# Optimization experiments

Hardware: AMD Instinct MI355X
Metric: run time of the kernel (lower is better)

Reference implementation:

```python
import jax, jax.numpy as jnp
import numpy as np

N_TOKENS = 4096
BATCH = 32


def setup_inputs() -> dict:
    key = jax.random.key(0)
    ks = jax.random.split(key, 9)
    n = N_TOKENS
    s = 0.02  # small init scale so exp(q*k) stays stable
    inp = {
        "x": jax.random.normal(ks[0], (BATCH, n), dtype=jnp.float32),
        "Wq": s * jax.random.normal(ks[1], (n, n), dtype=jnp.float32),
        "bq": jnp.zeros((n,), dtype=jnp.float32),
        "Wk": s * jax.random.normal(ks[2], (n, n), dtype=jnp.float32),
        "bk": jnp.zeros((n,), dtype=jnp.float32),
        "Wv": s * jax.random.normal(ks[3], (n, n), dtype=jnp.float32),
        "bv": jnp.zeros((n,), dtype=jnp.float32),
        "Wp": s * jax.random.normal(ks[4], (n, n), dtype=jnp.float32),
        "bp": jnp.zeros((n,), dtype=jnp.float32),
    }
    return inp


def reference(x, Wq, bq, Wk, bk, Wv, bv, Wp, bp):
    # Linear layers (torch convention: y = x @ W.T + b)
    q = x @ Wq.T + bq  # [b, n]
    k = x @ Wk.T + bk  # [b, n]
    v = x @ Wv.T + bv  # [b, n]
    # Rank-1 attention: scores[b,i,j] = q_i * k_j, softmax over j
    scores = q[:, :, None] * k[:, None, :]  # [b, n, n]
    w = jax.nn.softmax(scores, axis=2)
    attended = jnp.einsum('bij,bj->bi', w, v)  # [b, n]
    h = jax.nn.silu(x + attended)
    out = jax.nn.silu(h + h @ Wp.T + bp)
    return out
```

## Files before the change

kernel.cpp:

```cpp
#include <hip/hip_runtime.h>
#include <math.h>

#define N 4096
#define BATCH 32

#define NB 64
#define NP 9
#define QLO (-10.0f)
#define QBW 0.3125f
#define QINVBW 3.2f
#define NMOM (NB * 2 * NP)
#define NCHUNK 8

typedef short bf16x8 __attribute__((ext_vector_type(8)));
typedef float f32x4  __attribute__((ext_vector_type(4)));

static __device__ __forceinline__ float fast_exp2(float x) {
#if __has_builtin(__builtin_amdgcn_exp2f)
  return __builtin_amdgcn_exp2f(x);
#else
  return exp2f(x);
#endif
}

static __device__ __forceinline__ unsigned short f2bf_rne(float f) {
  unsigned int u = __float_as_uint(f);
  return (unsigned short)((u + 0x7FFFu + ((u >> 16) & 1u)) >> 16);
}
static __device__ __forceinline__ float bf2f(unsigned short h) {
  return __uint_as_float((unsigned int)h << 16);
}

__device__ const float c_invfact[NP] = {
  1.f, 1.f, 0.5f, 1.f/6.f, 1.f/24.f, 1.f/120.f, 1.f/720.f, 1.f/5040.f, 1.f/40320.f};

__global__ __launch_bounds__(256)
void prep_frags(const float* __restrict__ src, short* __restrict__ dst)
{
  int id = blockIdx.x * 256 + threadIdx.x;
  int narr = id >> 13;
  int rem  = id & 8191;
  int T = rem >> 6;
  int l = rem & 63;
  int b = (l & 15) | ((narr & 1) << 4);
  int k = T * 32 + ((l >> 4) << 3);
  const float* s = &src[(size_t)b * N + k];
  bf16x8 o;
  #pragma unroll
  for (int j = 0; j < 8; ++j) {
    float f = s[j];
    unsigned short h = f2bf_rne(f);
    if (narr >> 1) h = f2bf_rne(f - bf2f(h));
    o[j] = (short)h;
  }
  *(bf16x8*)&dst[(size_t)id * 8] = o;
}

template <int NSTEP, int NWAVES>
__device__ __forceinline__ void gemm_mfma_body(
    const float* __restrict__ W, const short* __restrict__ Xf,
    float* __restrict__ Y, int kbeg)
{
  const int t = threadIdx.x;
  const int w = t >> 6, l = t & 63;
  const int i0 = blockIdx.x * 16;

  const float* wrow = &W[(size_t)(i0 + (l & 15)) * N + kbeg + w * (NSTEP * 32) + ((l >> 4) << 3)];
  const short* bbase = Xf + (size_t)((kbeg >> 5) + w * NSTEP) * 512 + l * 8;

  f32x4 acc0 = {0.f, 0.f, 0.f, 0.f};
  f32x4 acc1 = {0.f, 0.f, 0.f, 0.f};

  #pragma unroll 4
  for (int s = 0; s < NSTEP; ++s) {
    float4 wa = *(const float4*)(wrow + s * 32);
    float4 wb = *(const float4*)(wrow + s * 32 + 4);
    bf16x8 bh0 = *(const bf16x8*)(bbase + (size_t)s * 512);
    bf16x8 bh1 = *(const bf16x8*)(bbase + (size_t)s * 512 + 65536);
    bf16x8 bl0 = *(const bf16x8*)(bbase + (size_t)s * 512 + 131072);
    bf16x8 bl1 = *(const bf16x8*)(bbase + (size_t)s * 512 + 196608);
    bf16x8 ah, al;
    #pragma unroll
    for (int e = 0; e < 8; ++e) {
      float x = (e < 4) ? ((const float*)&wa)[e] : ((const float*)&wb)[e - 4];
      unsigned int u = __float_as_uint(x);
      ah[e] = (short)(u >> 16);
      float r = x - __uint_as_float(u & 0xFFFF0000u);
      al[e] = (short)(__float_as_uint(r) >> 16);
    }
    acc0 = __builtin_amdgcn_mfma_f32_16x16x32_bf16(ah, bh0, acc0, 0, 0, 0);
    acc1 = __builtin_amdgcn_mfma_f32_16x16x32_bf16(ah, bh1, acc1, 0, 0, 0);
    acc0 = __builtin_amdgcn_mfma_f32_16x16x32_bf16(ah, bl0, acc0, 0, 0, 0);
    acc1 = __builtin_amdgcn_mfma_f32_16x16x32_bf16(ah, bl1, acc1, 0, 0, 0);
    acc0 = __builtin_amdgcn_mfma_f32_16x16x32_bf16(al, bh0, acc0, 0, 0, 0);
    acc1 = __builtin_amdgcn_mfma_f32_16x16x32_bf16(al, bh1, acc1, 0, 0, 0);
  }

  __shared__ float red[NWAVES][2][4][64];
  #pragma unroll
  for (int r = 0; r < 4; ++r) { red[w][0][r][l] = acc0[r]; red[w][1][r][l] = acc1[r]; }
  __syncthreads();

  #pragma unroll
  for (int e = t; e < 512; e += NWAVES * 64) {
    int b  = e >> 4;
    int il = e & 15;
    int n  = b >> 4;
    int lw = (b & 15) | ((il >> 2) << 4);
    int r  = il & 3;
    float v = 0.f;
    #pragma unroll
    for (int w2 = 0; w2 < NWAVES; ++w2) v += red[w2][n][r][lw];
    Y[(size_t)b * N + i0 + il] = v;
  }
}

__global__ __launch_bounds__(512) __attribute__((amdgpu_waves_per_eu(8)))
void gemm3(const short* __restrict__ Xf,
           const float* __restrict__ W0, const float* __restrict__ W1,
           const float* __restrict__ W2, float* __restrict__ GP)
{
  int m = blockIdx.y >> 1;
  const float* W = (m == 0) ? W0 : (m == 1) ? W1 : W2;
  gemm_mfma_body<8, 8>(W, Xf, GP + (size_t)blockIdx.y * (BATCH * N), (blockIdx.y & 1) * 2048);
}

__global__ __launch_bounds__(512) __attribute__((amdgpu_waves_per_eu(8)))
void gemm_p(const short* __restrict__ Hf, const float* __restrict__ W,
            float* __restrict__ GP)
{
  gemm_mfma_body<4, 8>(W, Hf, GP + (size_t)blockIdx.y * (BATCH * N), blockIdx.y * 1024);
}

__global__ __launch_bounds__(1024, 2)
void moments_a(const float* __restrict__ GP, const float* __restrict__ bk,
               const float* __restrict__ bv, float* __restrict__ P)
{
  const int b = blockIdx.x, chunk = blockIdx.y;
  const int t = threadIdx.x;
  const int wv = t >> 6, m = t & 63;

  __shared__ float ksm[512], vsm[512];
  {
    const float* GP2 = GP + (size_t)2 * BATCH * N;
    const float* GP3 = GP + (size_t)3 * BATCH * N;
    const float* GP4 = GP + (size_t)4 * BATCH * N;
    const float* GP5 = GP + (size_t)5 * BATCH * N;
    int col = chunk * 512 + (t & 511);
    size_t o = (size_t)b * N + col;
    if (t < 512) ksm[t] = GP2[o] + GP3[o] + bk[col];
    else         vsm[t & 511] = GP4[o] + GP5[o] + bv[col];
  }
  __syncthreads();

  const float gam = QLO + ((float)m + 0.5f) * QBW;
  const float gl2e = gam * 1.44269504f;
  float S[NP], T[NP];
  #pragma unroll
  for (int p = 0; p < NP; ++p) { S[p] = 0.f; T[p] = 0.f; }
  const int jb = wv * 32;
  #pragma unroll 4
  for (int jj = 0; jj < 32; ++jj) {
    float kj = ksm[jb + jj];
    float vj = vsm[jb + jj];
    float e = fast_exp2(gl2e * kj);
    float tp = e;
    S[0] += tp; T[0] = fmaf(tp, vj, T[0]);
    #pragma unroll
    for (int p = 1; p < NP; ++p) { tp *= kj; S[p] += tp; T[p] = fmaf(tp, vj, T[p]); }
  }
  __shared__ float red[16][NMOM];
  #pragma unroll
  for (int p = 0; p < NP; ++p) {
    red[wv][m * 18 + p] = S[p];
    red[wv][m * 18 + NP + p] = T[p];
  }
  __syncthreads();
  for (int e = t; e < NMOM; e += 1024) {
    float s = 0.f;
    #pragma unroll
    for (int w2 = 0; w2 < 16; ++w2) s += red[w2][e];
    P[((size_t)b * NCHUNK + chunk) * NMOM + e] = s;
  }
}

__global__ __launch_bounds__(256)
void attn_eval(const float* __restrict__ GP, const float* __restrict__ bq,
               const float* __restrict__ P, const float* __restrict__ x,
               float* __restrict__ h, short* __restrict__ Hf)
{
  const int b = blockIdx.x;
  const int i = blockIdx.y * 256 + threadIdx.x;
  __shared__ float cm[NMOM];
  for (int e = threadIdx.x; e < NMOM; e += 256) {
    float s = 0.f;
    #pragma unroll
    for (int c = 0; c < NCHUNK; ++c) s += P[((size_t)b * NCHUNK + c) * NMOM + e];
    int p = e % (2 * NP); if (p >= NP) p -= NP;
    cm[e] = s * c_invfact[p];
  }
  __syncthreads();
  size_t o = (size_t)b * N + i;
  float qv = GP[o] + GP[(size_t)BATCH * N + o] + bq[i];
  float qc = fminf(fmaxf(qv, QLO + 0.01f), -QLO - 0.01f);
  int m = (int)((qc - QLO) * QINVBW);
  float gam = QLO + ((float)m + 0.5f) * QBW;
  float d = qv - gam;
  const float* Sp = &cm[m * 18];
  float f = Sp[NP - 1], g = Sp[2 * NP - 1];
  #pragma unroll
  for (int p = NP - 2; p >= 0; --p) {
    f = fmaf(f, d, Sp[p]);
    g = fmaf(g, d, Sp[NP + p]);
  }
  float att = g / f;
  float z = x[o] + att;
  float hv = z / (1.f + fast_exp2(-1.44269504f * z));
  h[o] = hv;
  unsigned short hi = f2bf_rne(hv);
  unsigned short lo = f2bf_rne(hv - bf2f(hi));
  size_t base = (size_t)(b >> 4) * 65536 + (size_t)(i >> 5) * 512
              + (size_t)((b & 15) | (((i >> 3) & 3) << 4)) * 8 + (size_t)(i & 7);
  Hf[base] = (short)hi;
  Hf[base + 131072] = (short)lo;
}

__global__ __launch_bounds__(256)
void finalize_kernel(const float* __restrict__ h, const float* __restrict__ GP,
                     const float* __restrict__ bp, float* __restrict__ out)
{
  int idx = (blockIdx.x * 256 + threadIdx.x) * 4;
  int i = idx & (N - 1);
  const float* T0 = GP;
  const float* T1 = GP + (size_t)1 * BATCH * N;
  const float* T2 = GP + (size_t)2 * BATCH * N;
  const float* T3 = GP + (size_t)3 * BATCH * N;
  float4 hv = *(const float4*)&h[idx];
  float4 a  = *(const float4*)&T0[idx];
  float4 bb2 = *(const float4*)&T1[idx];
  float4 c  = *(const float4*)&T2[idx];
  float4 dd = *(const float4*)&T3[idx];
  float4 bb = *(const float4*)&bp[i];
  float4 z, o;
  z.x = hv.x + (a.x + bb2.x) + (c.x + dd.x) + bb.x;
  z.y = hv.y + (a.y + bb2.y) + (c.y + dd.y) + bb.y;
  z.z = hv.z + (a.z + bb2.z) + (c.z + dd.z) + bb.z;
  z.w = hv.w + (a.w + bb2.w) + (c.w + dd.w) + bb.w;
  o.x = z.x / (1.f + fast_exp2(-1.44269504f * z.x));
  o.y = z.y / (1.f + fast_exp2(-1.44269504f * z.y));
  o.z = z.z / (1.f + fast_exp2(-1.44269504f * z.z));
  o.w = z.w / (1.f + fast_exp2(-1.44269504f * z.w));
  *(float4*)&out[idx] = o;
}

extern "C" void kernel_launch(void* const* d_in, const int* in_sizes, int n_in,
                              void* d_out, int out_size, void* d_ws, size_t ws_size,
                              hipStream_t stream)
{
  const float* x  = (const float*)d_in[0];
  const float* Wq = (const float*)d_in[1];
  const float* bq = (const float*)d_in[2];
  const float* Wk = (const float*)d_in[3];
  const float* bk = (const float*)d_in[4];
  const float* Wv = (const float*)d_in[5];
  const float* bv = (const float*)d_in[6];
  const float* Wp = (const float*)d_in[7];
  const float* bp = (const float*)d_in[8];
  float* out = (float*)d_out;

  float* GP = (float*)d_ws;
  float* h  = GP + (size_t)6 * BATCH * N;
  short* Xf = (short*)(h + BATCH * N);
  short* Hf = Xf + 262144;
  float* P  = (float*)(Hf + 262144);

  prep_frags<<<dim3(128), 256, 0, stream>>>(x, Xf);
  gemm3<<<dim3(256, 6), 512, 0, stream>>>(Xf, Wq, Wk, Wv, GP);
  moments_a<<<dim3(BATCH, NCHUNK), 1024, 0, stream>>>(GP, bk, bv, P);
  attn_eval<<<dim3(BATCH, 16), 256, 0, stream>>>(GP, bq, P, x, h, Hf);
  gemm_p<<<dim3(256, 4), 512, 0, stream>>>(Hf, Wp, GP);
  finalize_kernel<<<dim3(128), 256, 0, stream>>>(h, GP, bp, out);
}
```

Baseline: 285.3 us.

## Double-buffer weight tiles via async global-to-LDS loads and drop split-K partials

The GEMM body now streams 16x256 float weight tiles into a double-buffered LDS staging area using global_load_lds async copies, so the next tile loads while MFMAs run on the current one. Each block covers a longer K range (full K for QKV, half K for the projection), which halves the number of blocks and partial outputs. The bias is fused into the GEMM epilogue, and the downstream kernels read finished q/k/v directly instead of summing split-K partials. The cost is less block-level parallelism (768 and 512 blocks), a __syncthreads on every tile, and the loss of the waves_per_eu hint.

```diff
diff --git a/kernel.cpp b/kernel.cpp
--- a/kernel.cpp
+++ b/kernel.cpp
@@ -33,6 +33,21 @@
 
 __device__ const float c_invfact[NP] = {
   1.f, 1.f, 0.5f, 1.f/6.f, 1.f/24.f, 1.f/120.f, 1.f/720.f, 1.f/5040.f, 1.f/40320.f};
+
+#if __has_builtin(__builtin_amdgcn_global_load_lds)
+#define HAVE_ASYNC_LDS 1
+#else
+#define HAVE_ASYNC_LDS 0
+#endif
+static __device__ __forceinline__ void async_cp16(const float* g, float* lds_base, int lane) {
+#if HAVE_ASYNC_LDS
+  __builtin_amdgcn_global_load_lds(
+      (const __attribute__((address_space(1))) void*)g,
+      (__attribute__((address_space(3))) void*)lds_base, 16, 0, 0);
+#else
+  ((float4*)lds_base)[lane] = *(const float4*)g;
+#endif
+}
 
 __global__ __launch_bounds__(256)
 void prep_frags(const float* __restrict__ src, short* __restrict__ dst)
@@ -56,33 +71,49 @@
   *(bf16x8*)&dst[(size_t)id * 8] = o;
 }
 
-template <int NSTEP, int NWAVES>
+template <int NTILE, bool FINAL>
 __device__ __forceinline__ void gemm_mfma_body(
     const float* __restrict__ W, const short* __restrict__ Xf,
-    float* __restrict__ Y, int kbeg)
-{
+    const float* __restrict__ bias, float* __restrict__ Y, int kbeg)
+{
+  __shared__ __align__(16) union GSm {
+    float stg[2][16][256];
+    float red[8][2][4][64];
+  } sm;
   const int t = threadIdx.x;
   const int w = t >> 6, l = t & 63;
   const int i0 = blockIdx.x * 16;
 
-  const float* wrow = &W[(size_t)(i0 + (l & 15)) * N + kbeg + w * (NSTEP * 32) + ((l >> 4) << 3)];
-  const short* bbase = Xf + (size_t)((kbeg >> 5) + w * NSTEP) * 512 + l * 8;
+  const float* gsrc0 = &W[(size_t)(i0 + 2 * w)     * N + kbeg + 4 * l];
+  const float* gsrc1 = &W[(size_t)(i0 + 2 * w + 1) * N + kbeg + 4 * l];
+  const short* bbase = Xf + (size_t)(kbeg >> 5) * 512 + l * 8;
 
   f32x4 acc0 = {0.f, 0.f, 0.f, 0.f};
   f32x4 acc1 = {0.f, 0.f, 0.f, 0.f};
 
-  #pragma unroll 4
-  for (int s = 0; s < NSTEP; ++s) {
-    float4 wa = *(const float4*)(wrow + s * 32);
-    float4 wb = *(const float4*)(wrow + s * 32 + 4);
-    bf16x8 bh0 = *(const bf16x8*)(bbase + (size_t)s * 512);
-    bf16x8 bh1 = *(const bf16x8*)(bbase + (size_t)s * 512 + 65536);
-    bf16x8 bl0 = *(const bf16x8*)(bbase + (size_t)s * 512 + 131072);
-    bf16x8 bl1 = *(const bf16x8*)(bbase + (size_t)s * 512 + 196608);
+  auto stage = [&](int buf, int tt) {
+    async_cp16(gsrc0 + tt * 256, &sm.stg[buf][2 * w][0], l);
+    async_cp16(gsrc1 + tt * 256, &sm.stg[buf][2 * w + 1][0], l);
+  };
+
+  stage(0, 0);
+  __syncthreads();
+  int buf = 0;
+  #pragma unroll 1
+  for (int tt = 0; tt < NTILE; ++tt) {
+    if (tt + 1 < NTILE) stage(buf ^ 1, tt + 1);
+    const short* bp = bbase + (size_t)(tt * 8 + w) * 512;
+    bf16x8 bh0 = *(const bf16x8*)(bp);
+    bf16x8 bh1 = *(const bf16x8*)(bp + 65536);
+    bf16x8 bl0 = *(const bf16x8*)(bp + 131072);
+    bf16x8 bl1 = *(const bf16x8*)(bp + 196608);
+    const float* ap = &sm.stg[buf][l & 15][w * 32 + ((l >> 4) << 3)];
+    float4 a0 = *(const float4*)ap;
+    float4 a1 = *(const float4*)(ap + 4);
     bf16x8 ah, al;
     #pragma unroll
     for (int e = 0; e < 8; ++e) {
-      float x = (e < 4) ? ((const float*)&wa)[e] : ((const float*)&wb)[e - 4];
+      float x = (e < 4) ? ((const float*)&a0)[e] : ((const float*)&a1)[e - 4];
       unsigned int u = __float_as_uint(x);
       ah[e] = (short)(u >> 16);
       float r = x - __uint_as_float(u & 0xFFFF0000u);
@@ -94,15 +125,16 @@
     acc1 = __builtin_amdgcn_mfma_f32_16x16x32_bf16(ah, bl1, acc1, 0, 0, 0);
     acc0 = __builtin_amdgcn_mfma_f32_16x16x32_bf16(al, bh0, acc0, 0, 0, 0);
     acc1 = __builtin_amdgcn_mfma_f32_16x16x32_bf16(al, bh1, acc1, 0, 0, 0);
-  }
-
-  __shared__ float red[NWAVES][2][4][64];
-  #pragma unroll
-  for (int r = 0; r < 4; ++r) { red[w][0][r][l] = acc0[r]; red[w][1][r][l] = acc1[r]; }
+    __syncthreads();
+    buf ^= 1;
+  }
+
+  #pragma unroll
+  for (int r = 0; r < 4; ++r) { sm.red[w][0][r][l] = acc0[r]; sm.red[w][1][r][l] = acc1[r]; }
   __syncthreads();
 
-  #pragma unroll
-  for (int e = t; e < 512; e += NWAVES * 64) {
+  {
+    int e  = t;
     int b  = e >> 4;
     int il = e & 15;
     int n  = b >> 4;
@@ -110,59 +142,50 @@
     int r  = il & 3;
     float v = 0.f;
     #pragma unroll
-    for (int w2 = 0; w2 < NWAVES; ++w2) v += red[w2][n][r][lw];
-    Y[(size_t)b * N + i0 + il] = v;
-  }
-}
-
-__global__ __launch_bounds__(512) __attribute__((amdgpu_waves_per_eu(8)))
+    for (int w2 = 0; w2 < 8; ++w2) v += sm.red[w2][n][r][lw];
+    int i = i0 + il;
+    Y[(size_t)b * N + i] = FINAL ? (v + bias[i]) : v;
+  }
+}
+
+__global__ __launch_bounds__(512)
 void gemm3(const short* __restrict__ Xf,
-           const float* __restrict__ W0, const float* __restrict__ W1,
-           const float* __restrict__ W2, float* __restrict__ GP)
-{
-  int m = blockIdx.y >> 1;
-  const float* W = (m == 0) ? W0 : (m == 1) ? W1 : W2;
-  gemm_mfma_body<8, 8>(W, Xf, GP + (size_t)blockIdx.y * (BATCH * N), (blockIdx.y & 1) * 2048);
-}
-
-__global__ __launch_bounds__(512) __attribute__((amdgpu_waves_per_eu(8)))
+           const float* __restrict__ W0, const float* __restrict__ b0, float* __restrict__ Y0,
+           const float* __restrict__ W1, const float* __restrict__ b1, float* __restrict__ Y1,
+           const float* __restrict__ W2, const float* __restrict__ b2, float* __restrict__ Y2)
+{
+  const float* W = W0; const float* bias = b0; float* Y = Y0;
+  if (blockIdx.y == 1) { W = W1; bias = b1; Y = Y1; }
+  else if (blockIdx.y == 2) { W = W2; bias = b2; Y = Y2; }
+  gemm_mfma_body<16, true>(W, Xf, bias, Y, 0);
+}
+
+__global__ __launch_bounds__(512)
 void gemm_p(const short* __restrict__ Hf, const float* __restrict__ W,
             float* __restrict__ GP)
 {
-  gemm_mfma_body<4, 8>(W, Hf, GP + (size_t)blockIdx.y * (BATCH * N), blockIdx.y * 1024);
+  gemm_mfma_body<8, false>(W, Hf, nullptr, GP + (size_t)blockIdx.y * (BATCH * N),
+                           blockIdx.y * 2048);
 }
 
 __global__ __launch_bounds__(1024, 2)
-void moments_a(const float* __restrict__ GP, const float* __restrict__ bk,
-               const float* __restrict__ bv, float* __restrict__ P)
+void moments_a(const float* __restrict__ kk, const float* __restrict__ vv,
+               float* __restrict__ P)
 {
   const int b = blockIdx.x, chunk = blockIdx.y;
   const int t = threadIdx.x;
   const int wv = t >> 6, m = t & 63;
-
-  __shared__ float ksm[512], vsm[512];
-  {
-    const float* GP2 = GP + (size_t)2 * BATCH * N;
-    const float* GP3 = GP + (size_t)3 * BATCH * N;
-    const float* GP4 = GP + (size_t)4 * BATCH * N;
-    const float* GP5 = GP + (size_t)5 * BATCH * N;
-    int col = chunk * 512 + (t & 511);
-    size_t o = (size_t)b * N + col;
-    if (t < 512) ksm[t] = GP2[o] + GP3[o] + bk[col];
-    else         vsm[t & 511] = GP4[o] + GP5[o] + bv[col];
-  }
-  __syncthreads();
-
   const float gam = QLO + ((float)m + 0.5f) * QBW;
   const float gl2e = gam * 1.44269504f;
   float S[NP], T[NP];
   #pragma unroll
   for (int p = 0; p < NP; ++p) { S[p] = 0.f; T[p] = 0.f; }
-  const int jb = wv * 32;
+  const float* kb = &kk[(size_t)b * N + chunk * 512 + wv * 32];
+  const float* vb = &vv[(size_t)b * N + chunk * 512 + wv * 32];
   #pragma unroll 4
   for (int jj = 0; jj < 32; ++jj) {
-    float kj = ksm[jb + jj];
-    float vj = vsm[jb + jj];
+    float kj = kb[jj];
+    float vj = vb[jj];
     float e = fast_exp2(gl2e * kj);
     float tp = e;
     S[0] += tp; T[0] = fmaf(tp, vj, T[0]);
@@ -185,9 +208,9 @@
 }
 
 __global__ __launch_bounds__(256)
-void attn_eval(const float* __restrict__ GP, const float* __restrict__ bq,
-               const float* __restrict__ P, const float* __restrict__ x,
-               float* __restrict__ h, short* __restrict__ Hf)
+void attn_eval(const float* __restrict__ q, const float* __restrict__ P,
+               const float* __restrict__ x, float* __restrict__ h,
+               short* __restrict__ Hf)
 {
   const int b = blockIdx.x;
   const int i = blockIdx.y * 256 + threadIdx.x;
@@ -201,7 +224,7 @@
   }
   __syncthreads();
   size_t o = (size_t)b * N + i;
-  float qv = GP[o] + GP[(size_t)BATCH * N + o] + bq[i];
+  float qv = q[o];
   float qc = fminf(fmaxf(qv, QLO + 0.01f), -QLO - 0.01f);
   int m = (int)((qc - QLO) * QINVBW);
   float gam = QLO + ((float)m + 0.5f) * QBW;
@@ -233,19 +256,15 @@
   int i = idx & (N - 1);
   const float* T0 = GP;
   const float* T1 = GP + (size_t)1 * BATCH * N;
-  const float* T2 = GP + (size_t)2 * BATCH * N;
-  const float* T3 = GP + (size_t)3 * BATCH * N;
   float4 hv = *(const float4*)&h[idx];
   float4 a  = *(const float4*)&T0[idx];
-  float4 bb2 = *(const float4*)&T1[idx];
-  float4 c  = *(const float4*)&T2[idx];
-  float4 dd = *(const float4*)&T3[idx];
+  float4 bt = *(const float4*)&T1[idx];
   float4 bb = *(const float4*)&bp[i];
   float4 z, o;
-  z.x = hv.x + (a.x + bb2.x) + (c.x + dd.x) + bb.x;
-  z.y = hv.y + (a.y + bb2.y) + (c.y + dd.y) + bb.y;
-  z.z = hv.z + (a.z + bb2.z) + (c.z + dd.z) + bb.z;
-  z.w = hv.w + (a.w + bb2.w) + (c.w + dd.w) + bb.w;
+  z.x = hv.x + (a.x + bt.x) + bb.x;
+  z.y = hv.y + (a.y + bt.y) + bb.y;
+  z.z = hv.z + (a.z + bt.z) + bb.z;
+  z.w = hv.w + (a.w + bt.w) + bb.w;
   o.x = z.x / (1.f + fast_exp2(-1.44269504f * z.x));
   o.y = z.y / (1.f + fast_exp2(-1.44269504f * z.y));
   o.z = z.z / (1.f + fast_exp2(-1.44269504f * z.z));
@@ -269,15 +288,18 @@
   float* out = (float*)d_out;
 
   float* GP = (float*)d_ws;
-  float* h  = GP + (size_t)6 * BATCH * N;
+  float* q  = GP + (size_t)2 * BATCH * N;
+  float* kk = q  + BATCH * N;
+  float* vv = kk + BATCH * N;
+  float* h  = vv + BATCH * N;
   short* Xf = (short*)(h + BATCH * N);
   short* Hf = Xf + 262144;
   float* P  = (float*)(Hf + 262144);
 
   prep_frags<<<dim3(128), 256, 0, stream>>>(x, Xf);
-  gemm3<<<dim3(256, 6), 512, 0, stream>>>(Xf, Wq, Wk, Wv, GP);
-  moments_a<<<dim3(BATCH, NCHUNK), 1024, 0, stream>>>(GP, bk, bv, P);
-  attn_eval<<<dim3(BATCH, 16), 256, 0, stream>>>(GP, bq, P, x, h, Hf);
-  gemm_p<<<dim3(256, 4), 512, 0, stream>>>(Hf, Wp, GP);
+  gemm3<<<dim3(256, 3), 512, 0, stream>>>(Xf, Wq, bq, q, Wk, bk, kk, Wv, bv, vv);
+  moments_a<<<dim3(BATCH, NCHUNK), 1024, 0, stream>>>(kk, vv, P);
+  attn_eval<<<dim3(BATCH, 16), 256, 0, stream>>>(q, P, x, h, Hf);
+  gemm_p<<<dim3(256, 2), 512, 0, stream>>>(Hf, Wp, GP);
   finalize_kernel<<<dim3(128), 256, 0, stream>>>(h, GP, bp, out);
 }
```

Measured after the change: 273.1 us. 1.04x faster.
